# Kernel tuning notes

Hardware: AMD Instinct MI355X
Metric: run time of the kernel (lower is better)

The kernel has to match this reference:

```python
import jax, jax.numpy as jnp
import numpy as np

DEPTH, FEAT, HID = 20, 2048, 1024
HALF = FEAT // 2
CLAMP = 2.0
TWO_OVER_PI = 0.6366197723675814  # FrEIA's 0.636619772


def setup_inputs() -> dict:
    key = jax.random.key(0)
    ks = jax.random.split(key, 9)
    x = jax.random.normal(ks[0], (4096, FEAT), dtype=jnp.float32)
    # FrEIA PermuteRandom: numpy permutation seeded with layer index k
    perms = jnp.asarray(
        np.stack([np.random.RandomState(k).permutation(FEAT) for k in range(DEPTH)]),
        dtype=jnp.int32,
    )
    def w(k, shape):  # module reinits all params as 0.01*randn
        return 0.01 * jax.random.normal(k, shape, dtype=jnp.float32)
    return {
        "x": x, "perms": perms,
        "s1_w1": w(ks[1], (DEPTH, HALF, HID)), "s1_b1": w(ks[2], (DEPTH, HID)),
        "s1_w2": w(ks[3], (DEPTH, HID, FEAT)), "s1_b2": w(ks[4], (DEPTH, FEAT)),
        "s2_w1": w(ks[5], (DEPTH, HALF, HID)), "s2_b1": w(ks[6], (DEPTH, HID)),
        "s2_w2": w(ks[7], (DEPTH, HID, FEAT)), "s2_b2": w(ks[8], (DEPTH, FEAT)),
    }


def _subnet(x, w1, b1, w2, b2):
    h = x @ w1 + b1
    h = jnp.where(h >= 0, h, 0.01 * h)  # LeakyReLU(negative_slope=0.01)
    return h @ w2 + b2


def reference(x, perms, s1_w1, s1_b1, s1_w2, s1_b2, s2_w1, s2_b1, s2_w2, s2_b2):
    def body(carry, xs):
        z, jac = carry
        perm, w1a, b1a, w1b, b1b, w2a, b2a, w2b, b2b = xs
        z = z[:, perm]                       # PermuteRandom
        x1, x2 = z[:, :HALF], z[:, HALF:]    # GLOW coupling split
        r2 = _subnet(x2, w2a, b2a, w2b, b2b)  # [B, FEAT] -> (s2, t2)
        e2 = CLAMP * TWO_OVER_PI * jnp.arctan(r2[:, :HALF] / CLAMP)
        y1 = jnp.exp(e2) * x1 + r2[:, HALF:]
        r1 = _subnet(y1, w1a, b1a, w1b, b1b)  # (s1, t1)
        e1 = CLAMP * TWO_OVER_PI * jnp.arctan(r1[:, :HALF] / CLAMP)
        y2 = jnp.exp(e1) * x2 + r1[:, HALF:]
        jac = jac + e1.sum(-1) + e2.sum(-1)  # log|det J| per sample
        return (jnp.concatenate([y1, y2], axis=-1), jac), None

    jac0 = jnp.zeros(x.shape[0], dtype=x.dtype)
    (z, jac), _ = jax.lax.scan(
        body, (x, jac0),
        (perms, s1_w1, s1_b1, s1_w2, s1_b2, s2_w1, s2_b1, s2_w2, s2_b2),
    )
    return z, jac
```

## Files before the change

kernel.cpp:

```cpp
#include <hip/hip_runtime.h>
#include <stdint.h>

#define DEPTH 20
#define FEAT  2048
#define HALF  1024
#define HID   1024
#define MROWS 4096

typedef __bf16 bf16x8 __attribute__((ext_vector_type(8)));
typedef float  f32x4  __attribute__((ext_vector_type(4)));
typedef unsigned int u32x4 __attribute__((ext_vector_type(4)));

__device__ __forceinline__ unsigned short f2bf(float f) {
  union { float f; unsigned int u; } v; v.f = f;
  unsigned int u = v.u + 0x7fffu + ((v.u >> 16) & 1u);
  return (unsigned short)(u >> 16);
}

__device__ __forceinline__ void async_cp16(unsigned short* lds, const unsigned short* g) {
  __builtin_amdgcn_global_load_lds(
      (const __attribute__((address_space(1))) void*)g,
      (__attribute__((address_space(3))) void*)lds, 16, 0, 0);
}

__device__ __forceinline__ bf16x8 lds_ld8(const unsigned short* p) {
  return __builtin_bit_cast(bf16x8, *(const u32x4*)p);
}

__global__ void wcvt_k(const float* __restrict__ s2w1, const float* __restrict__ s2w2,
                       const float* __restrict__ s1w1, const float* __restrict__ s1w2,
                       unsigned short* __restrict__ w2a, unsigned short* __restrict__ w2b,
                       unsigned short* __restrict__ w1a, unsigned short* __restrict__ w1b) {
  const float* src; unsigned short* dst; int N, pp;
  switch (blockIdx.z) {
    case 0:  src = s2w1; dst = w2a; N = 1024; pp = 0; break;
    case 1:  src = s2w2; dst = w2b; N = 2048; pp = 1; break;
    case 2:  src = s1w1; dst = w1a; N = 1024; pp = 0; break;
    default: src = s1w2; dst = w1b; N = 2048; pp = 1; break;
  }
  int nb = blockIdx.x * 32;
  if (nb >= N) return;
  int kb = blockIdx.y * 32;
  __shared__ float t[32][33];
  int tx = threadIdx.x, ty = threadIdx.y;
#pragma unroll
  for (int s = 0; s < 4; ++s)
    t[ty + 8*s][tx] = src[(size_t)(kb + ty + 8*s) * N + nb + tx];
  __syncthreads();
  int pbase = pp ? (nb < 1024 ? 2*nb : 2*(nb - 1024) + 32) : nb;
#pragma unroll
  for (int s = 0; s < 4; ++s) {
    int nl = ty + 8*s;
    dst[(size_t)(pbase + nl) * 1024 + kb + tx] = f2bf(t[tx][nl]);
  }
}

__device__ __forceinline__ int porig(int p) {
  int g = p >> 6, o = p & 63;
  return (o < 32) ? (g*32 + o) : (1024 + g*32 + (o - 32));
}

__global__ void bias_k(const float* __restrict__ s2b1, const float* __restrict__ s2b2,
                       const float* __restrict__ s1b1, const float* __restrict__ s1b2,
                       float* __restrict__ b2a, float* __restrict__ b2b,
                       float* __restrict__ b1a, float* __restrict__ b1b) {
  int i = blockIdx.x * 256 + threadIdx.x;
  if (i < 1024)      b2a[i] = s2b1[i];
  else if (i < 3072) { int p = i - 1024; b2b[p] = s2b2[porig(p)]; }
  else if (i < 4096) b1a[i - 3072] = s1b1[i - 3072];
  else               { int p = i - 4096; b1b[p] = s1b2[porig(p)]; }
}

__global__ void permute_k(const float* __restrict__ z, const int* __restrict__ perm,
                          float* __restrict__ x1f, float* __restrict__ x2f,
                          unsigned short* __restrict__ x2b) {
  int c = blockIdx.x * 256 + threadIdx.x;
  int row0 = blockIdx.y * 8;
  int pc = perm[c];
#pragma unroll
  for (int r = 0; r < 8; ++r) {
    int row = row0 + r;
    float v = z[row * FEAT + pc];
    if (c < HALF) {
      x1f[row * HALF + c] = v;
    } else {
      x2f[row * HALF + c - HALF] = v;
      x2b[row * HALF + c - HALF] = f2bf(v);
    }
  }
}

template<int EPI>
__launch_bounds__(256)
__global__ void gemm_k(const unsigned short* __restrict__ A,
                       const unsigned short* __restrict__ Bt,
                       const float* __restrict__ bias,
                       const float* __restrict__ xin,
                       float* __restrict__ yout,
                       unsigned short* __restrict__ ybf,
                       float* __restrict__ jac,
                       unsigned short* __restrict__ hout) {
  __shared__ unsigned short As[128 * 32];
  __shared__ unsigned short Bs[128 * 32];
  const int tid  = threadIdx.x;
  const int wave = tid >> 6, lane = tid & 63;
  const int quad = lane >> 4, l15 = lane & 15;
  const int wy = wave >> 1, wx = wave & 1;
  const int bm = blockIdx.y * 128;
  const int bn = blockIdx.x * 128;
  const int K = 1024;

  f32x4 acc[4][4];
#pragma unroll
  for (int i = 0; i < 4; ++i)
#pragma unroll
    for (int j = 0; j < 4; ++j)
#pragma unroll
      for (int r = 0; r < 4; ++r) acc[i][j][r] = 0.0f;

  const int gbase = wave * 64 + lane;

  for (int kt = 0; kt < 32; ++kt) {
    const int k0 = kt * 32;
#pragma unroll
    for (int i = 0; i < 2; ++i) {
      int g  = i * 256 + gbase;
      int r  = g >> 2, kg = g & 3;
      async_cp16(&As[(i * 256 + wave * 64) * 8], A  + (size_t)(bm + r) * K + k0 + kg * 8);
      async_cp16(&Bs[(i * 256 + wave * 64) * 8], Bt + (size_t)(bn + r) * K + k0 + kg * 8);
    }
    asm volatile("s_waitcnt vmcnt(0)" ::: "memory");
    __syncthreads();

    bf16x8 af[4], bf[4];
#pragma unroll
    for (int i = 0; i < 4; ++i)
      af[i] = lds_ld8(&As[(wy * 64 + i * 16 + l15) * 32 + quad * 8]);
#pragma unroll
    for (int j = 0; j < 4; ++j)
      bf[j] = lds_ld8(&Bs[(wx * 64 + j * 16 + l15) * 32 + quad * 8]);
#pragma unroll
    for (int i = 0; i < 4; ++i)
#pragma unroll
      for (int j = 0; j < 4; ++j)
        acc[i][j] = __builtin_amdgcn_mfma_f32_16x16x32_bf16(af[i], bf[j], acc[i][j], 0, 0, 0);
    __syncthreads();
  }

  if (EPI == 0) {
    const int ldo = gridDim.x * 128;
#pragma unroll
    for (int j = 0; j < 4; ++j) {
      int col = bn + wx * 64 + j * 16 + l15;
      float bj = bias[col];
#pragma unroll
      for (int i = 0; i < 4; ++i) {
#pragma unroll
        for (int r = 0; r < 4; ++r) {
          int row = bm + wy * 64 + i * 16 + quad * 4 + r;
          float v = acc[i][j][r] + bj;
          v = v >= 0.0f ? v : 0.01f * v;
          hout[(size_t)row * ldo + col] = f2bf(v);
        }
      }
    }
  } else {
    const int g = (bn >> 6) + wx;
#pragma unroll
    for (int i = 0; i < 4; ++i) {
      float esum[4] = {0.0f, 0.0f, 0.0f, 0.0f};
#pragma unroll
      for (int j = 0; j < 2; ++j) {
        int pe = bn + wx * 64 + j * 16 + l15;
        float be = bias[pe];
        float ba = bias[pe + 32];
        int xcol = g * 32 + j * 16 + l15;
#pragma unroll
        for (int r = 0; r < 4; ++r) {
          int row = bm + wy * 64 + i * 16 + quad * 4 + r;
          float re = acc[i][j][r] + be;
          float ra = acc[i][j + 2][r] + ba;
          float e  = 1.2732395447351628f * atanf(0.5f * re);
          float y  = __expf(e) * xin[(size_t)row * HALF + xcol] + ra;
          yout[(size_t)row * FEAT + xcol] = y;
          if (ybf) ybf[(size_t)row * HALF + xcol] = f2bf(y);
          esum[r] += e;
        }
      }
#pragma unroll
      for (int r = 0; r < 4; ++r) {
        float v = esum[r];
        v += __shfl_xor(v, 1);
        v += __shfl_xor(v, 2);
        v += __shfl_xor(v, 4);
        v += __shfl_xor(v, 8);
        if (l15 == 0) {
          int row = bm + wy * 64 + i * 16 + quad * 4 + r;
          atomicAdd(&jac[row], v);
        }
      }
    }
  }
}

__global__ void jcopy_k(const float* __restrict__ jac, float* __restrict__ out) {
  int i = blockIdx.x * 256 + threadIdx.x;
  if (i < 4096) out[i] = jac[i];
}

extern "C" void kernel_launch(void* const* d_in, const int* in_sizes, int n_in,
                              void* d_out, int out_size, void* d_ws, size_t ws_size,
                              hipStream_t stream) {
  const float* x     = (const float*)d_in[0];
  const int*   perms = (const int*)d_in[1];
  const float* s1w1  = (const float*)d_in[2];
  const float* s1b1  = (const float*)d_in[3];
  const float* s1w2  = (const float*)d_in[4];
  const float* s1b2  = (const float*)d_in[5];
  const float* s2w1  = (const float*)d_in[6];
  const float* s2b1  = (const float*)d_in[7];
  const float* s2w2  = (const float*)d_in[8];
  const float* s2b2  = (const float*)d_in[9];
  float* out = (float*)d_out;

  size_t off = 0;
  char* base = (char*)d_ws;
  auto alloc = [&](size_t bytes) {
    void* r = base + off;
    off += (bytes + 255) & ~(size_t)255;
    return r;
  };
  float*          x1f = (float*)alloc((size_t)MROWS * HALF * 4);
  float*          x2f = (float*)alloc((size_t)MROWS * HALF * 4);
  unsigned short* x2b = (unsigned short*)alloc((size_t)MROWS * HALF * 2);
  unsigned short* y1b = (unsigned short*)alloc((size_t)MROWS * HALF * 2);
  unsigned short* hb  = (unsigned short*)alloc((size_t)MROWS * HID * 2);
  float*          zbuf= (float*)alloc((size_t)MROWS * FEAT * 4);
  unsigned short* w2a = (unsigned short*)alloc((size_t)HALF * HID * 2);
  unsigned short* w2b = (unsigned short*)alloc((size_t)FEAT * HID * 2);
  unsigned short* w1a = (unsigned short*)alloc((size_t)HALF * HID * 2);
  unsigned short* w1b = (unsigned short*)alloc((size_t)FEAT * HID * 2);
  float* b2a = (float*)alloc(1024 * 4);
  float* b2b = (float*)alloc(2048 * 4);
  float* b1a = (float*)alloc(1024 * 4);
  float* b1b = (float*)alloc(2048 * 4);
  float* jac = (float*)alloc(4096 * 4);

  hipMemsetAsync(jac, 0, 4096 * 4, stream);

  for (int d = 0; d < DEPTH; ++d) {
    wcvt_k<<<dim3(64, 32, 4), dim3(32, 8), 0, stream>>>(
        s2w1 + (size_t)d * HALF * HID, s2w2 + (size_t)d * HID * FEAT,
        s1w1 + (size_t)d * HALF * HID, s1w2 + (size_t)d * HID * FEAT,
        w2a, w2b, w1a, w1b);
    bias_k<<<24, 256, 0, stream>>>(s2b1 + (size_t)d * HID, s2b2 + (size_t)d * FEAT,
                                   s1b1 + (size_t)d * HID, s1b2 + (size_t)d * FEAT,
                                   b2a, b2b, b1a, b1b);
    const float* zsrc = (d == 0) ? x : zbuf;
    permute_k<<<dim3(8, 512), 256, 0, stream>>>(zsrc, perms + (size_t)d * FEAT, x1f, x2f, x2b);

    float* zdst = (d == DEPTH - 1) ? out : zbuf;
    gemm_k<0><<<dim3(8, 32), 256, 0, stream>>>(x2b, w2a, b2a, nullptr, nullptr, nullptr, nullptr, hb);
    gemm_k<1><<<dim3(16, 32), 256, 0, stream>>>(hb, w2b, b2b, x1f, zdst, y1b, jac, nullptr);
    gemm_k<0><<<dim3(8, 32), 256, 0, stream>>>(y1b, w1a, b1a, nullptr, nullptr, nullptr, nullptr, hb);
    gemm_k<1><<<dim3(16, 32), 256, 0, stream>>>(hb, w1b, b1b, x2f, zdst + HALF, nullptr, jac, nullptr);
  }
  jcopy_k<<<16, 256, 0, stream>>>(jac, out + (size_t)MROWS * FEAT);
}
```

Before: 3.760 ms.

## Pipeline GEMM K-loop with 4-stage LDS buffers and batch weight prep

The GEMM main loop moves from a single LDS buffer with a full wait each step to a 4-deep ring of buffers. Loads are issued three tiles ahead and waited on with partial vmcnt counts, which hides global latency behind MFMA work. Weight and bias conversion for all depths now runs once up front in a single launch each instead of per layer, cutting launch count at the cost of a much larger workspace. The permute now reads input rows contiguously and scatters through an inverse permutation, trading gathered reads for scattered writes.

```diff
diff --git a/kernel.cpp b/kernel.cpp
--- a/kernel.cpp
+++ b/kernel.cpp
@@ -27,16 +27,17 @@
   return __builtin_bit_cast(bf16x8, *(const u32x4*)p);
 }
 
-__global__ void wcvt_k(const float* __restrict__ s2w1, const float* __restrict__ s2w2,
-                       const float* __restrict__ s1w1, const float* __restrict__ s1w2,
-                       unsigned short* __restrict__ w2a, unsigned short* __restrict__ w2b,
-                       unsigned short* __restrict__ w1a, unsigned short* __restrict__ w1b) {
+__global__ void wcvt_all_k(const float* __restrict__ s2w1, const float* __restrict__ s2w2,
+                           const float* __restrict__ s1w1, const float* __restrict__ s1w2,
+                           unsigned short* __restrict__ wall) {
+  const int d = blockIdx.z >> 2, m = blockIdx.z & 3;
   const float* src; unsigned short* dst; int N, pp;
-  switch (blockIdx.z) {
-    case 0:  src = s2w1; dst = w2a; N = 1024; pp = 0; break;
-    case 1:  src = s2w2; dst = w2b; N = 2048; pp = 1; break;
-    case 2:  src = s1w1; dst = w1a; N = 1024; pp = 0; break;
-    default: src = s1w2; dst = w1b; N = 2048; pp = 1; break;
+  const size_t L = (size_t)6 * 1024 * 1024;
+  switch (m) {
+    case 0:  src = s2w1 + (size_t)d*HALF*HID; dst = wall + d*L;                 N = 1024; pp = 0; break;
+    case 1:  src = s2w2 + (size_t)d*HID*FEAT; dst = wall + d*L + 1024*1024;     N = 2048; pp = 1; break;
+    case 2:  src = s1w1 + (size_t)d*HALF*HID; dst = wall + d*L + 3*1024*1024;   N = 1024; pp = 0; break;
+    default: src = s1w2 + (size_t)d*HID*FEAT; dst = wall + d*L + 4*1024*1024;   N = 2048; pp = 1; break;
   }
   int nb = blockIdx.x * 32;
   if (nb >= N) return;
@@ -60,36 +61,47 @@
   return (o < 32) ? (g*32 + o) : (1024 + g*32 + (o - 32));
 }
 
-__global__ void bias_k(const float* __restrict__ s2b1, const float* __restrict__ s2b2,
-                       const float* __restrict__ s1b1, const float* __restrict__ s1b2,
-                       float* __restrict__ b2a, float* __restrict__ b2b,
-                       float* __restrict__ b1a, float* __restrict__ b1b) {
+__global__ void bias_all_k(const float* __restrict__ s2b1, const float* __restrict__ s2b2,
+                           const float* __restrict__ s1b1, const float* __restrict__ s1b2,
+                           float* __restrict__ ball) {
   int i = blockIdx.x * 256 + threadIdx.x;
-  if (i < 1024)      b2a[i] = s2b1[i];
-  else if (i < 3072) { int p = i - 1024; b2b[p] = s2b2[porig(p)]; }
-  else if (i < 4096) b1a[i - 3072] = s1b1[i - 3072];
-  else               { int p = i - 4096; b1b[p] = s1b2[porig(p)]; }
-}
-
-__global__ void permute_k(const float* __restrict__ z, const int* __restrict__ perm,
+  int d = i / 6144, o = i % 6144;
+  float v;
+  if (o < 1024)      v = s2b1[d*1024 + o];
+  else if (o < 3072) v = s2b2[d*2048 + porig(o - 1024)];
+  else if (o < 4096) v = s1b1[d*1024 + (o - 3072)];
+  else               v = s1b2[d*2048 + porig(o - 4096)];
+  ball[i] = v;
+}
+
+__global__ void iperm_k(const int* __restrict__ perms, int* __restrict__ iperm) {
+  int i = blockIdx.x * 256 + threadIdx.x;
+  int d = i >> 11, c = i & 2047;
+  iperm[(d << 11) + perms[i]] = c;
+}
+
+__global__ void permute_k(const float* __restrict__ z, const int* __restrict__ iperm,
                           float* __restrict__ x1f, float* __restrict__ x2f,
                           unsigned short* __restrict__ x2b) {
   int c = blockIdx.x * 256 + threadIdx.x;
   int row0 = blockIdx.y * 8;
-  int pc = perm[c];
+  int ic = iperm[c];
+  bool lo = ic < HALF;
+  int off = lo ? ic : ic - HALF;
 #pragma unroll
   for (int r = 0; r < 8; ++r) {
     int row = row0 + r;
-    float v = z[row * FEAT + pc];
-    if (c < HALF) {
-      x1f[row * HALF + c] = v;
+    float v = z[(size_t)row * FEAT + c];
+    if (lo) {
+      x1f[(size_t)row * HALF + off] = v;
     } else {
-      x2f[row * HALF + c - HALF] = v;
-      x2b[row * HALF + c - HALF] = f2bf(v);
+      x2f[(size_t)row * HALF + off] = v;
+      x2b[(size_t)row * HALF + off] = f2bf(v);
     }
   }
 }
 
+#define NKT 32
 template<int EPI>
 __launch_bounds__(256)
 __global__ void gemm_k(const unsigned short* __restrict__ A,
@@ -100,8 +112,8 @@
                        unsigned short* __restrict__ ybf,
                        float* __restrict__ jac,
                        unsigned short* __restrict__ hout) {
-  __shared__ unsigned short As[128 * 32];
-  __shared__ unsigned short Bs[128 * 32];
+  __shared__ unsigned short As[4][128 * 32];
+  __shared__ unsigned short Bs[4][128 * 32];
   const int tid  = threadIdx.x;
   const int wave = tid >> 6, lane = tid & 63;
   const int quad = lane >> 4, l15 = lane & 15;
@@ -119,36 +131,53 @@
       for (int r = 0; r < 4; ++r) acc[i][j][r] = 0.0f;
 
   const int gbase = wave * 64 + lane;
-
-  for (int kt = 0; kt < 32; ++kt) {
+  const int g0 = gbase, g1 = 256 + gbase;
+  const int r0 = g0 >> 2, kg0 = g0 & 3;
+  const int r1 = g1 >> 2, kg1 = g1 & 3;
+  const unsigned short* a0 = A  + (size_t)(bm + r0) * K + kg0 * 8;
+  const unsigned short* a1 = A  + (size_t)(bm + r1) * K + kg1 * 8;
+  const unsigned short* b0 = Bt + (size_t)(bn + r0) * K + kg0 * 8;
+  const unsigned short* b1 = Bt + (size_t)(bn + r1) * K + kg1 * 8;
+  const int ldsoff = wave * 64 * 8;
+
+  auto stage = [&](int kt) {
+    const int buf = kt & 3;
     const int k0 = kt * 32;
-#pragma unroll
-    for (int i = 0; i < 2; ++i) {
-      int g  = i * 256 + gbase;
-      int r  = g >> 2, kg = g & 3;
-      async_cp16(&As[(i * 256 + wave * 64) * 8], A  + (size_t)(bm + r) * K + k0 + kg * 8);
-      async_cp16(&Bs[(i * 256 + wave * 64) * 8], Bt + (size_t)(bn + r) * K + k0 + kg * 8);
-    }
-    asm volatile("s_waitcnt vmcnt(0)" ::: "memory");
-    __syncthreads();
-
+    async_cp16(&As[buf][ldsoff],            a0 + k0);
+    async_cp16(&As[buf][256 * 8 + ldsoff],  a1 + k0);
+    async_cp16(&Bs[buf][ldsoff],            b0 + k0);
+    async_cp16(&Bs[buf][256 * 8 + ldsoff],  b1 + k0);
+  };
+
+  stage(0); stage(1); stage(2);
+
+  for (int kt = 0; kt < NKT; ++kt) {
+    if (kt + 3 < NKT) stage(kt + 3);
+    if (kt < NKT - 3)      asm volatile("s_waitcnt vmcnt(12)" ::: "memory");
+    else if (kt == NKT-3)  asm volatile("s_waitcnt vmcnt(8)"  ::: "memory");
+    else if (kt == NKT-2)  asm volatile("s_waitcnt vmcnt(4)"  ::: "memory");
+    else                   asm volatile("s_waitcnt vmcnt(0)"  ::: "memory");
+    asm volatile("s_barrier" ::: "memory");
+
+    const unsigned short* as = As[kt & 3];
+    const unsigned short* bs = Bs[kt & 3];
     bf16x8 af[4], bf[4];
 #pragma unroll
     for (int i = 0; i < 4; ++i)
-      af[i] = lds_ld8(&As[(wy * 64 + i * 16 + l15) * 32 + quad * 8]);
+      af[i] = lds_ld8(&as[(wy * 64 + i * 16 + l15) * 32 + quad * 8]);
 #pragma unroll
     for (int j = 0; j < 4; ++j)
-      bf[j] = lds_ld8(&Bs[(wx * 64 + j * 16 + l15) * 32 + quad * 8]);
+      bf[j] = lds_ld8(&bs[(wx * 64 + j * 16 + l15) * 32 + quad * 8]);
 #pragma unroll
     for (int i = 0; i < 4; ++i)
 #pragma unroll
       for (int j = 0; j < 4; ++j)
         acc[i][j] = __builtin_amdgcn_mfma_f32_16x16x32_bf16(af[i], bf[j], acc[i][j], 0, 0, 0);
-    __syncthreads();
+    if (kt < NKT - 1) asm volatile("s_barrier" ::: "memory");
   }
 
   if (EPI == 0) {
-    const int ldo = gridDim.x * 128;
+    const int ldo = 1024;
 #pragma unroll
     for (int j = 0; j < 4; ++j) {
       int col = bn + wx * 64 + j * 16 + l15;
@@ -230,34 +259,36 @@
     off += (bytes + 255) & ~(size_t)255;
     return r;
   };
-  float*          x1f = (float*)alloc((size_t)MROWS * HALF * 4);
-  float*          x2f = (float*)alloc((size_t)MROWS * HALF * 4);
-  unsigned short* x2b = (unsigned short*)alloc((size_t)MROWS * HALF * 2);
-  unsigned short* y1b = (unsigned short*)alloc((size_t)MROWS * HALF * 2);
-  unsigned short* hb  = (unsigned short*)alloc((size_t)MROWS * HID * 2);
-  float*          zbuf= (float*)alloc((size_t)MROWS * FEAT * 4);
-  unsigned short* w2a = (unsigned short*)alloc((size_t)HALF * HID * 2);
-  unsigned short* w2b = (unsigned short*)alloc((size_t)FEAT * HID * 2);
-  unsigned short* w1a = (unsigned short*)alloc((size_t)HALF * HID * 2);
-  unsigned short* w1b = (unsigned short*)alloc((size_t)FEAT * HID * 2);
-  float* b2a = (float*)alloc(1024 * 4);
-  float* b2b = (float*)alloc(2048 * 4);
-  float* b1a = (float*)alloc(1024 * 4);
-  float* b1b = (float*)alloc(2048 * 4);
-  float* jac = (float*)alloc(4096 * 4);
+  float*          x1f  = (float*)alloc((size_t)MROWS * HALF * 4);
+  float*          x2f  = (float*)alloc((size_t)MROWS * HALF * 4);
+  unsigned short* x2b  = (unsigned short*)alloc((size_t)MROWS * HALF * 2);
+  unsigned short* y1b  = (unsigned short*)alloc((size_t)MROWS * HALF * 2);
+  unsigned short* hb   = (unsigned short*)alloc((size_t)MROWS * HID * 2);
+  float*          zbuf = (float*)alloc((size_t)MROWS * FEAT * 4);
+  unsigned short* wall = (unsigned short*)alloc((size_t)DEPTH * 6 * 1024 * 1024 * 2);
+  float*          ball = (float*)alloc((size_t)DEPTH * 6144 * 4);
+  int*            ipm  = (int*)alloc((size_t)DEPTH * FEAT * 4);
+  float*          jac  = (float*)alloc(4096 * 4);
 
   hipMemsetAsync(jac, 0, 4096 * 4, stream);
 
+  iperm_k<<<DEPTH * FEAT / 256, 256, 0, stream>>>(perms, ipm);
+  wcvt_all_k<<<dim3(64, 32, DEPTH * 4), dim3(32, 8), 0, stream>>>(s2w1, s2w2, s1w1, s1w2, wall);
+  bias_all_k<<<DEPTH * 6144 / 256, 256, 0, stream>>>(s2b1, s2b2, s1b1, s1b2, ball);
+
+  const size_t L = (size_t)6 * 1024 * 1024;
   for (int d = 0; d < DEPTH; ++d) {
-    wcvt_k<<<dim3(64, 32, 4), dim3(32, 8), 0, stream>>>(
-        s2w1 + (size_t)d * HALF * HID, s2w2 + (size_t)d * HID * FEAT,
-        s1w1 + (size_t)d * HALF * HID, s1w2 + (size_t)d * HID * FEAT,
-        w2a, w2b, w1a, w1b);
-    bias_k<<<24, 256, 0, stream>>>(s2b1 + (size_t)d * HID, s2b2 + (size_t)d * FEAT,
-                                   s1b1 + (size_t)d * HID, s1b2 + (size_t)d * FEAT,
-                                   b2a, b2b, b1a, b1b);
+    const unsigned short* w2a = wall + d * L;
+    const unsigned short* w2b = wall + d * L + 1024 * 1024;
+    const unsigned short* w1a = wall + d * L + 3 * 1024 * 1024;
+    const unsigned short* w1b = wall + d * L + 4 * 1024 * 1024;
+    const float* b2a = ball + d * 6144;
+    const float* b2b = ball + d * 6144 + 1024;
+    const float* b1a = ball + d * 6144 + 3072;
+    const float* b1b = ball + d * 6144 + 4096;
+
     const float* zsrc = (d == 0) ? x : zbuf;
-    permute_k<<<dim3(8, 512), 256, 0, stream>>>(zsrc, perms + (size_t)d * FEAT, x1f, x2f, x2b);
+    permute_k<<<dim3(8, 512), 256, 0, stream>>>(zsrc, ipm + (size_t)d * FEAT, x1f, x2f, x2b);
 
     float* zdst = (d == DEPTH - 1) ? out : zbuf;
     gemm_k<0><<<dim3(8, 32), 256, 0, stream>>>(x2b, w2a, b2a, nullptr, nullptr, nullptr, nullptr, hb);
```

New measurement: 4.986 ms. 32.6% more time.
